# Optimization experiments

Hardware: AMD Instinct MI355X
Metric: run time of the kernel (lower is better)

## Reference

```python
import jax, jax.numpy as jnp
import numpy as np

BLOCK_DIM = 32
INPUT_DIM = 1024
N_BLOCKS = INPUT_DIM // BLOCK_DIM  # 32
HIDDEN = 2 * BLOCK_DIM             # 64
GAPS = [1, 32]                     # block_dim**i for i in range(num_layers=2)


def setup_inputs() -> dict:
    key = jax.random.key(0)
    ks = jax.random.split(key, 9)
    s = 1.0 / np.sqrt(BLOCK_DIM)
    sh = 1.0 / np.sqrt(HIDDEN)
    return {
        "x": jax.random.normal(ks[0], (16384, INPUT_DIM), dtype=jnp.float32),
        # facto net 0: BlockLinear(32, 32, 64) -> ELU -> BlockLinear(32, 64, 32)
        "W1a": jax.random.uniform(ks[1], (N_BLOCKS, BLOCK_DIM, HIDDEN), jnp.float32, -s, s),
        "b1a": jax.random.uniform(ks[2], (N_BLOCKS, HIDDEN), jnp.float32, -s, s),
        "W2a": jax.random.uniform(ks[3], (N_BLOCKS, HIDDEN, BLOCK_DIM), jnp.float32, -sh, sh),
        "b2a": jax.random.uniform(ks[4], (N_BLOCKS, BLOCK_DIM), jnp.float32, -sh, sh),
        # facto net 1
        "W1b": jax.random.uniform(ks[5], (N_BLOCKS, BLOCK_DIM, HIDDEN), jnp.float32, -s, s),
        "b1b": jax.random.uniform(ks[6], (N_BLOCKS, HIDDEN), jnp.float32, -s, s),
        "W2b": jax.random.uniform(ks[7], (N_BLOCKS, HIDDEN, BLOCK_DIM), jnp.float32, -sh, sh),
        "b2b": jax.random.uniform(ks[8], (N_BLOCKS, BLOCK_DIM), jnp.float32, -sh, sh),
    }


def _block_res_mlp(x, W1, b1, W2, b2):
    # x: (bs, input_dim) -> (n_blocks, bs, block_dim)
    bs = x.shape[0]
    xb = x.reshape(bs, N_BLOCKS, BLOCK_DIM).transpose(1, 0, 2)
    h = jax.nn.elu(jnp.einsum('nbi,nio->nbo', xb, W1) + b1[:, None, :])
    h = jnp.einsum('nbi,nio->nbo', h, W2) + b2[:, None, :]
    yb = h + xb  # residual
    return yb.transpose(1, 0, 2).reshape(bs, -1)


def reference(x, W1a, b1a, W2a, b2a, W1b, b1b, W2b, b2b):
    bs = x.shape[0]
    params = [(W1a, b1a, W2a, b2a), (W1b, b1b, W2b, b2b)]
    y = x
    for gap, (W1, b1, W2, b2) in zip(GAPS, params):
        # strided mixing permutation before the block MLP
        y = y.reshape(-1, BLOCK_DIM, gap).transpose(0, 2, 1).reshape(bs, -1)
        y = _block_res_mlp(y, W1, b1, W2, b2)
        # inverse permutation
        y = y.reshape(-1, gap, BLOCK_DIM).transpose(0, 2, 1)
    return y.reshape(bs, -1)
```

## Files before the change

kernel.cpp:

```cpp
#include <hip/hip_runtime.h>


typedef unsigned short u16t;
typedef __bf16 bf16x8 __attribute__((ext_vector_type(8)));
typedef float f32x4 __attribute__((ext_vector_type(4)));

#define LDC 34

__device__ __forceinline__ u16t f2b(float f) {
  union { float f; unsigned u; } v; v.f = f;
  unsigned r = v.u + 0x7FFFu + ((v.u >> 16) & 1u);
  return (u16t)(r >> 16);
}
__device__ __forceinline__ float b2f(u16t h) {
  union { unsigned u; float f; } v; v.u = ((unsigned)h) << 16;
  return v.f;
}

union BF { u16t us[8]; bf16x8 v; };

__global__ __launch_bounds__(256) void pack_weights(
    const float* __restrict__ W1a, const float* __restrict__ W2a,
    const float* __restrict__ W1b, const float* __restrict__ W2b,
    u16t* __restrict__ pW1, u16t* __restrict__ pW2) {
  int tidg = blockIdx.x * 256 + threadIdx.x;
  int tensor = tidg >> 14;
  int r  = tidg & 16383;
  int L  = r >> 13;
  int r2 = r & 8191;
  int n    = r2 >> 8;
  int f    = (r2 >> 6) & 3;
  int lane = r2 & 63;
  int q = lane >> 4, t = lane & 15;

  union { u16t us[8]; uint4 v; } w;
  if (tensor == 0) {
    const float* src = L ? W1b : W1a;
#pragma unroll
    for (int j = 0; j < 8; j++) {
      int kz = L ? (4 * j + q) : (q * 8 + j);
      w.us[j] = f2b(src[n * 2048 + kz * 64 + f * 16 + t]);
    }
    *(uint4*)(pW1 + (size_t)((L * 32 + n) * 2048 + f * 512 + lane * 8)) = w.v;
  } else {
    const float* src = L ? W2b : W2a;
    int kc = f >> 1, c2 = f & 1;
#pragma unroll
    for (int j = 0; j < 8; j++) {
      int H = kc * 32 + (j >> 2) * 16 + q * 4 + (j & 3);
      w.us[j] = f2b(src[n * 2048 + H * 32 + c2 * 16 + t]);
    }
    *(uint4*)(pW2 + (size_t)((L * 32 + n) * 2048 + f * 512 + lane * 8)) = w.v;
  }
}

template <int L>
__device__ __forceinline__ void compute_layer(
    const bf16x8* afr, unsigned* __restrict__ tile32,
    const u16t* __restrict__ pW1, const u16t* __restrict__ pW2,
    const float* __restrict__ b1, const float* __restrict__ b2,
    const bf16x8* E, int w, int q, int t, int lane) {
  const f32x4 zf = {0.f, 0.f, 0.f, 0.f};
#pragma unroll
  for (int u = 0; u < 8; u++) {
    const int n = w * 8 + u;
    const int base = (L * 32 + n) * 2048 + lane * 8;
    bf16x8 w1f[4], w2f[4];
#pragma unroll
    for (int c = 0; c < 4; c++) {
      w1f[c] = *(const bf16x8*)(pW1 + base + c * 512);
      w2f[c] = *(const bf16x8*)(pW2 + base + c * 512);
    }
    f32x4 accH[4];
#pragma unroll
    for (int c = 0; c < 4; c++)
      accH[c] = __builtin_amdgcn_mfma_f32_16x16x32_bf16(w1f[c], afr[u], zf, 0, 0, 0);

    BF hf[2];
#pragma unroll
    for (int c = 0; c < 4; c++) {
      union { float4 v; float f[4]; } B1;
      B1.v = *(const float4*)(b1 + n * 64 + c * 16 + q * 4);
#pragma unroll
      for (int r = 0; r < 4; r++) {
        float vv = accH[c][r] + B1.f[r];
        vv = vv > 0.f ? vv : (__expf(vv) - 1.f);
        hf[c >> 1].us[(c & 1) * 4 + r] = f2b(vv);
      }
    }

#pragma unroll
    for (int c2 = 0; c2 < 2; c2++) {
      f32x4 acc = __builtin_amdgcn_mfma_f32_16x16x32_bf16(E[c2], afr[u], zf, 0, 0, 0);
      acc = __builtin_amdgcn_mfma_f32_16x16x32_bf16(w2f[c2],     hf[0].v, acc, 0, 0, 0);
      acc = __builtin_amdgcn_mfma_f32_16x16x32_bf16(w2f[2 + c2], hf[1].v, acc, 0, 0, 0);
      union { float4 v; float f[4]; } B2;
      B2.v = *(const float4*)(b2 + n * 32 + c2 * 16 + q * 4);
      const int phys = ((c2 * 16 + q * 4) + 4 * (n >> 2)) & 31;
      const int a32 = (((n * 16 + t) * LDC) + phys) >> 1;
      unsigned d0 = (unsigned)f2b(acc[0] + B2.f[0]) | ((unsigned)f2b(acc[1] + B2.f[1]) << 16);
      unsigned d1 = (unsigned)f2b(acc[2] + B2.f[2]) | ((unsigned)f2b(acc[3] + B2.f[3]) << 16);
      tile32[a32] = d0;
      tile32[a32 + 1] = d1;
    }
  }
}

__global__ __launch_bounds__(256, 4) void mixer_kernel(
    const float* __restrict__ x,
    const float* __restrict__ b1a, const float* __restrict__ b2a,
    const float* __restrict__ b1b, const float* __restrict__ b2b,
    const u16t* __restrict__ pW1, const u16t* __restrict__ pW2,
    float* __restrict__ out) {
  __shared__ unsigned tile32[(32 * 16 * LDC) / 2];
  const u16t* tile16 = (const u16t*)tile32;
  const int tid = threadIdx.x, w = tid >> 6, lane = tid & 63;
  const int q = lane >> 4, t = lane & 15;
  const int r0 = blockIdx.x * 16;

  bf16x8 afr[8];
#pragma unroll
  for (int u = 0; u < 8; u++) {
    const int n = w * 8 + u;
    const float* gp = x + (size_t)(r0 + t) * 1024 + n * 32 + q * 8;
    float4 v0 = *(const float4*)gp;
    float4 v1 = *(const float4*)(gp + 4);
    BF a;
    a.us[0] = f2b(v0.x); a.us[1] = f2b(v0.y); a.us[2] = f2b(v0.z); a.us[3] = f2b(v0.w);
    a.us[4] = f2b(v1.x); a.us[5] = f2b(v1.y); a.us[6] = f2b(v1.z); a.us[7] = f2b(v1.w);
    afr[u] = a.v;
  }

  bf16x8 E[2];
#pragma unroll
  for (int c2 = 0; c2 < 2; c2++) {
    BF e;
#pragma unroll
    for (int j = 0; j < 8; j++)
      e.us[j] = (q * 8 + j == c2 * 16 + t) ? (u16t)0x3F80 : (u16t)0;
    E[c2] = e.v;
  }

  compute_layer<0>(afr, tile32, pW1, pW2, b1a, b2a, E, w, q, t, lane);
  __syncthreads();

  BF zfr[8];
#pragma unroll
  for (int j = 0; j < 8; j++) {
    const int k = 4 * j + q;
    const int rb = (k * 16 + t) * LDC;
#pragma unroll
    for (int g = 0; g < 2; g++) {
      const int pg = (8 * w + 4 * g + 4 * j) & 31;
      const unsigned d0 = tile32[(rb + pg) >> 1];
      const unsigned d1 = tile32[((rb + pg) >> 1) + 1];
      zfr[4 * g + 0].us[j] = (u16t)(d0 & 0xFFFF);
      zfr[4 * g + 1].us[j] = (u16t)(d0 >> 16);
      zfr[4 * g + 2].us[j] = (u16t)(d1 & 0xFFFF);
      zfr[4 * g + 3].us[j] = (u16t)(d1 >> 16);
    }
  }

#pragma unroll
  for (int c2 = 0; c2 < 2; c2++) {
    BF e;
#pragma unroll
    for (int j = 0; j < 8; j++)
      e.us[j] = (4 * j + q == c2 * 16 + t) ? (u16t)0x3F80 : (u16t)0;
    E[c2] = e.v;
  }
  __syncthreads();

  compute_layer<1>((const bf16x8*)zfr, tile32, pW1, pW2, b1b, b2b, E, w, q, t, lane);
  __syncthreads();

  const int row = lane & 15, l4 = lane >> 4;
#pragma unroll
  for (int i = 0; i < 16; i++) {
    const int F0 = 4 * (i * 16 + w * 4 + l4);
    const int bn = F0 & 31, cc = F0 >> 5;
    const int phys = (cc + 4 * (bn >> 2)) & 31;
    union { float4 v; float f[4]; } o;
#pragma unroll
    for (int e = 0; e < 4; e++)
      o.f[e] = b2f(tile16[((bn + e) * 16 + row) * LDC + phys]);
    *(float4*)(out + (size_t)(r0 + row) * 1024 + F0) = o.v;
  }
}

extern "C" void kernel_launch(void* const* d_in, const int* in_sizes, int n_in,
                              void* d_out, int out_size, void* d_ws, size_t ws_size,
                              hipStream_t stream) {
  const float* x   = (const float*)d_in[0];
  const float* W1a = (const float*)d_in[1];
  const float* b1a = (const float*)d_in[2];
  const float* W2a = (const float*)d_in[3];
  const float* b2a = (const float*)d_in[4];
  const float* W1b = (const float*)d_in[5];
  const float* b1b = (const float*)d_in[6];
  const float* W2b = (const float*)d_in[7];
  const float* b2b = (const float*)d_in[8];
  float* out = (float*)d_out;

  u16t* pW1 = (u16t*)d_ws;
  u16t* pW2 = pW1 + 131072;

  const int rows = in_sizes[0] / 1024;

  pack_weights<<<128, 256, 0, stream>>>(W1a, W2a, W1b, W2b, pW1, pW2);
  mixer_kernel<<<rows / 16, 256, 0, stream>>>(x, b1a, b2a, b1b, b2b, pW1, pW2, out);
}
```

Measured before the change: 180.5 us.

## Stream x loads per block, fold biases into MFMA accumulators, use packed bf16 converts

```diff
diff --git a/kernel.cpp b/kernel.cpp
--- a/kernel.cpp
+++ b/kernel.cpp
@@ -3,6 +3,7 @@
 
 typedef unsigned short u16t;
 typedef __bf16 bf16x8 __attribute__((ext_vector_type(8)));
+typedef __bf16 bf16x2 __attribute__((ext_vector_type(2)));
 typedef float f32x4 __attribute__((ext_vector_type(4)));
 
 #define LDC 34
@@ -16,8 +17,17 @@
   union { unsigned u; float f; } v; v.u = ((unsigned)h) << 16;
   return v.f;
 }
-
-union BF { u16t us[8]; bf16x8 v; };
+__device__ __forceinline__ unsigned pk2(float a, float b) {
+#if __has_builtin(__builtin_amdgcn_cvt_pk_bf16_f32)
+  union { bf16x2 v; unsigned u; } cv;
+  cv.v = __builtin_amdgcn_cvt_pk_bf16_f32(a, b);
+  return cv.u;
+#else
+  return (unsigned)f2b(a) | ((unsigned)f2b(b) << 16);
+#endif
+}
+
+union BF { u16t us[8]; unsigned d[4]; bf16x8 v; };
 
 __global__ __launch_bounds__(256) void pack_weights(
     const float* __restrict__ W1a, const float* __restrict__ W2a,
@@ -56,57 +66,74 @@
 
 template <int L>
 __device__ __forceinline__ void compute_layer(
-    const bf16x8* afr, unsigned* __restrict__ tile32,
+    const float* __restrict__ xg, const bf16x8* zfr,
+    unsigned* __restrict__ tile32,
     const u16t* __restrict__ pW1, const u16t* __restrict__ pW2,
     const float* __restrict__ b1, const float* __restrict__ b2,
-    const bf16x8* E, int w, int q, int t, int lane) {
-  const f32x4 zf = {0.f, 0.f, 0.f, 0.f};
+    const bf16x8* E, int w, int q, int t) {
+  const int lane8 = (q * 16 + t) * 8;
+  float4 v0, v1;
+  if (L == 0) {
+    const float* gp = xg + (w * 8) * 32 + q * 8;
+    v0 = *(const float4*)gp;
+    v1 = *(const float4*)(gp + 4);
+  }
 #pragma unroll
   for (int u = 0; u < 8; u++) {
     const int n = w * 8 + u;
-    const int base = (L * 32 + n) * 2048 + lane * 8;
+    bf16x8 af;
+    if (L == 0) {
+      BF a;
+      a.d[0] = pk2(v0.x, v0.y); a.d[1] = pk2(v0.z, v0.w);
+      a.d[2] = pk2(v1.x, v1.y); a.d[3] = pk2(v1.z, v1.w);
+      af = a.v;
+      if (u < 7) {
+        const float* gp = xg + (n + 1) * 32 + q * 8;
+        v0 = *(const float4*)gp;
+        v1 = *(const float4*)(gp + 4);
+      }
+    } else {
+      af = zfr[u];
+    }
+
+    const int base = (L * 32 + n) * 2048 + lane8;
     bf16x8 w1f[4], w2f[4];
 #pragma unroll
     for (int c = 0; c < 4; c++) {
       w1f[c] = *(const bf16x8*)(pW1 + base + c * 512);
       w2f[c] = *(const bf16x8*)(pW2 + base + c * 512);
     }
-    f32x4 accH[4];
-#pragma unroll
-    for (int c = 0; c < 4; c++)
-      accH[c] = __builtin_amdgcn_mfma_f32_16x16x32_bf16(w1f[c], afr[u], zf, 0, 0, 0);
 
     BF hf[2];
 #pragma unroll
     for (int c = 0; c < 4; c++) {
-      union { float4 v; float f[4]; } B1;
-      B1.v = *(const float4*)(b1 + n * 64 + c * 16 + q * 4);
-#pragma unroll
-      for (int r = 0; r < 4; r++) {
-        float vv = accH[c][r] + B1.f[r];
-        vv = vv > 0.f ? vv : (__expf(vv) - 1.f);
-        hf[c >> 1].us[(c & 1) * 4 + r] = f2b(vv);
-      }
+      float4 B1 = *(const float4*)(b1 + n * 64 + c * 16 + q * 4);
+      f32x4 bc = {B1.x, B1.y, B1.z, B1.w};
+      f32x4 acc = __builtin_amdgcn_mfma_f32_16x16x32_bf16(w1f[c], af, bc, 0, 0, 0);
+      float e0 = acc[0] > 0.f ? acc[0] : (__expf(acc[0]) - 1.f);
+      float e1 = acc[1] > 0.f ? acc[1] : (__expf(acc[1]) - 1.f);
+      float e2 = acc[2] > 0.f ? acc[2] : (__expf(acc[2]) - 1.f);
+      float e3 = acc[3] > 0.f ? acc[3] : (__expf(acc[3]) - 1.f);
+      hf[c >> 1].d[(c & 1) * 2 + 0] = pk2(e0, e1);
+      hf[c >> 1].d[(c & 1) * 2 + 1] = pk2(e2, e3);
     }
 
 #pragma unroll
     for (int c2 = 0; c2 < 2; c2++) {
-      f32x4 acc = __builtin_amdgcn_mfma_f32_16x16x32_bf16(E[c2], afr[u], zf, 0, 0, 0);
+      float4 B2 = *(const float4*)(b2 + n * 32 + c2 * 16 + q * 4);
+      f32x4 bc = {B2.x, B2.y, B2.z, B2.w};
+      f32x4 acc = __builtin_amdgcn_mfma_f32_16x16x32_bf16(E[c2], af, bc, 0, 0, 0);
       acc = __builtin_amdgcn_mfma_f32_16x16x32_bf16(w2f[c2],     hf[0].v, acc, 0, 0, 0);
       acc = __builtin_amdgcn_mfma_f32_16x16x32_bf16(w2f[2 + c2], hf[1].v, acc, 0, 0, 0);
-      union { float4 v; float f[4]; } B2;
-      B2.v = *(const float4*)(b2 + n * 32 + c2 * 16 + q * 4);
       const int phys = ((c2 * 16 + q * 4) + 4 * (n >> 2)) & 31;
       const int a32 = (((n * 16 + t) * LDC) + phys) >> 1;
-      unsigned d0 = (unsigned)f2b(acc[0] + B2.f[0]) | ((unsigned)f2b(acc[1] + B2.f[1]) << 16);
-      unsigned d1 = (unsigned)f2b(acc[2] + B2.f[2]) | ((unsigned)f2b(acc[3] + B2.f[3]) << 16);
-      tile32[a32] = d0;
-      tile32[a32 + 1] = d1;
-    }
-  }
-}
-
-__global__ __launch_bounds__(256, 4) void mixer_kernel(
+      tile32[a32]     = pk2(acc[0], acc[1]);
+      tile32[a32 + 1] = pk2(acc[2], acc[3]);
+    }
+  }
+}
+
+__global__ __launch_bounds__(256) void mixer_kernel(
     const float* __restrict__ x,
     const float* __restrict__ b1a, const float* __restrict__ b2a,
     const float* __restrict__ b1b, const float* __restrict__ b2b,
@@ -117,19 +144,7 @@
   const int tid = threadIdx.x, w = tid >> 6, lane = tid & 63;
   const int q = lane >> 4, t = lane & 15;
   const int r0 = blockIdx.x * 16;
-
-  bf16x8 afr[8];
-#pragma unroll
-  for (int u = 0; u < 8; u++) {
-    const int n = w * 8 + u;
-    const float* gp = x + (size_t)(r0 + t) * 1024 + n * 32 + q * 8;
-    float4 v0 = *(const float4*)gp;
-    float4 v1 = *(const float4*)(gp + 4);
-    BF a;
-    a.us[0] = f2b(v0.x); a.us[1] = f2b(v0.y); a.us[2] = f2b(v0.z); a.us[3] = f2b(v0.w);
-    a.us[4] = f2b(v1.x); a.us[5] = f2b(v1.y); a.us[6] = f2b(v1.z); a.us[7] = f2b(v1.w);
-    afr[u] = a.v;
-  }
+  const float* xg = x + (size_t)(r0 + t) * 1024;
 
   bf16x8 E[2];
 #pragma unroll
@@ -141,7 +156,7 @@
     E[c2] = e.v;
   }
 
-  compute_layer<0>(afr, tile32, pW1, pW2, b1a, b2a, E, w, q, t, lane);
+  compute_layer<0>(xg, nullptr, tile32, pW1, pW2, b1a, b2a, E, w, q, t);
   __syncthreads();
 
   BF zfr[8];
@@ -171,7 +186,7 @@
   }
   __syncthreads();
 
-  compute_layer<1>((const bf16x8*)zfr, tile32, pW1, pW2, b1b, b2b, E, w, q, t, lane);
+  compute_layer<1>(nullptr, (const bf16x8*)zfr, tile32, pW1, pW2, b1b, b2b, E, w, q, t);
   __syncthreads();
 
   const int row = lane & 15, l4 = lane >> 4;
```

Result: faster. 175.0 us (-3.0%).
